# Optimization experiments

Measured on AMD Instinct MI355X. Metric: run time of the kernel, lower is better.

The kernel has to match this reference:

```python
import jax, jax.numpy as jnp
import numpy as np

B, C, H, W = 8, 256, 128, 128
CQ = C // 8  # query/key channel dim = 32


def setup_inputs() -> dict:
    key = jax.random.key(0)
    ks = jax.random.split(key, 8)
    s = 0.05
    return {
        "x": jax.random.normal(ks[0], (B, C, H, W), jnp.float32),
        "Wq": jax.random.normal(ks[1], (CQ, C), jnp.float32) * s,
        "bq": jax.random.normal(ks[2], (CQ,), jnp.float32) * s,
        "Wk": jax.random.normal(ks[3], (CQ, C), jnp.float32) * s,
        "bk": jax.random.normal(ks[4], (CQ,), jnp.float32) * s,
        "Wv": jax.random.normal(ks[5], (C, C), jnp.float32) * s,
        "bv": jax.random.normal(ks[6], (C,), jnp.float32) * s,
        "gamma": jax.random.normal(ks[7], (1,), jnp.float32),
    }


def reference(x, Wq, bq, Wk, bk, Wv, bv, gamma):
    b, c, h, w = x.shape
    # 1x1 convs == channel-mixing einsums
    q = jnp.einsum('oc,bchw->bohw', Wq, x) + bq[None, :, None, None]   # [B,CQ,H,W]
    k = jnp.einsum('oc,bchw->bohw', Wk, x) + bk[None, :, None, None]   # [B,CQ,H,W]
    v = jnp.einsum('oc,bchw->bohw', Wv, x) + bv[None, :, None, None]   # [B,C,H,W]
    # energy along height: for each column w, attend over rows g; -inf on diagonal
    eH = jnp.einsum('bohw,bogw->bhwg', q, k)                            # [B,H,W,H]
    diag = jnp.eye(h, dtype=bool)                                       # h==g
    eH = jnp.where(diag[None, :, None, :], -jnp.inf, eH)
    # energy along width: for each row h, attend over columns g
    eW = jnp.einsum('bohw,bohg->bhwg', q, k)                            # [B,H,W,W]
    att = jax.nn.softmax(jnp.concatenate([eH, eW], axis=-1), axis=-1)   # [B,H,W,H+W]
    aH, aW = att[..., :h], att[..., h:]
    outH = jnp.einsum('bhwg,bcgw->bchw', aH, v)
    outW = jnp.einsum('bhwg,bchg->bchw', aW, v)
    return gamma[0] * (outH + outW) + x
```

## Files before the change

kernel.cpp:

```cpp
#include <hip/hip_runtime.h>
#include <math.h>

#define B 8
#define C 256
#define CQ 32
#define H 128
#define W 128
#define P (H*W)

typedef unsigned short ushortT;
typedef __attribute__((ext_vector_type(8))) short bf16x8;
typedef __attribute__((ext_vector_type(4))) float f32x4;

__device__ __forceinline__ float bf2f(ushortT u) {
    union { unsigned int i; float f; } v; v.i = ((unsigned int)u) << 16; return v.f;
}
__device__ __forceinline__ ushortT f2bf(float f) {
    union { float f; unsigned int i; } v; v.f = f;
    unsigned int u = v.i;
    unsigned int r = (u + 0x7FFFu + ((u >> 16) & 1u)) >> 16;
    return (ushortT)r;
}

__global__ void pack_kernel(
    const float* __restrict__ Wq, const float* __restrict__ bq,
    const float* __restrict__ Wk, const float* __restrict__ bk,
    const float* __restrict__ Wv, const float* __restrict__ bv,
    ushortT* __restrict__ Wall, float* __restrict__ biasAll)
{
    const int t = threadIdx.x;
    if (blockIdx.x == 80) {
        for (int i = t; i < 320; i += 256) {
            float bv_;
            if (i < 32)       bv_ = bq[i];
            else if (i < 64)  bv_ = bk[i - 32];
            else              bv_ = bv[i - 64];
            biasAll[i] = bv_;
        }
        return;
    }
    int g = blockIdx.x * 256 + t;
    int idx4 = g * 4;
    int row = idx4 >> 8, col = idx4 & 255;
    const float* src;
    if (row < 32)       src = Wq + (size_t)row * 256 + col;
    else if (row < 64)  src = Wk + (size_t)(row - 32) * 256 + col;
    else                src = Wv + (size_t)(row - 64) * 256 + col;
    float4 v4 = *(const float4*)src;
    ushort4 u;
    u.x = f2bf(v4.x); u.y = f2bf(v4.y); u.z = f2bf(v4.z); u.w = f2bf(v4.w);
    *(ushort4*)(Wall + idx4) = u;
}

__global__ __launch_bounds__(256) void proj_mfma(
    const float* __restrict__ x, const ushortT* __restrict__ Wall,
    const float* __restrict__ biasAll,
    ushortT* __restrict__ qb, ushortT* __restrict__ kb, ushortT* __restrict__ vb)
{
    __shared__ ushortT Xs[64][264];
    const int t  = threadIdx.x;
    const int p0 = blockIdx.x * 64;
    const int b  = blockIdx.y;

    {
        const float* xb = x + (size_t)b * C * P + p0;
        int c = t >> 4, pq = (t & 15) * 4;
        #pragma unroll
        for (int i = 0; i < 16; i++) {
            int ci = c + i * 16;
            float4 v4 = *(const float4*)(xb + (size_t)ci * P + pq);
            Xs[pq + 0][ci] = f2bf(v4.x);
            Xs[pq + 1][ci] = f2bf(v4.y);
            Xs[pq + 2][ci] = f2bf(v4.z);
            Xs[pq + 3][ci] = f2bf(v4.w);
        }
    }
    __syncthreads();

    const int wid = t >> 6, lane = t & 63;
    const int lrow = lane & 15, lk = (lane >> 4) * 8;

    f32x4 acc[5][4];
    #pragma unroll
    for (int mi = 0; mi < 5; mi++)
        #pragma unroll
        for (int ni = 0; ni < 4; ni++)
            acc[mi][ni] = (f32x4){0.f, 0.f, 0.f, 0.f};

    const ushortT* wbase = Wall + (size_t)(wid * 80 + lrow) * 256 + lk;

    #pragma unroll
    for (int kk = 0; kk < 8; kk++) {
        bf16x8 a[5], bfr[4];
        #pragma unroll
        for (int mi = 0; mi < 5; mi++)
            a[mi] = *(const bf16x8*)(wbase + mi * 16 * 256 + kk * 32);
        #pragma unroll
        for (int ni = 0; ni < 4; ni++)
            bfr[ni] = *(const bf16x8*)&Xs[ni * 16 + lrow][kk * 32 + lk];
        #pragma unroll
        for (int mi = 0; mi < 5; mi++)
            #pragma unroll
            for (int ni = 0; ni < 4; ni++)
                acc[mi][ni] = __builtin_amdgcn_mfma_f32_16x16x32_bf16(
                    a[mi], bfr[ni], acc[mi][ni], 0, 0, 0);
    }

    const int orow0 = wid * 80 + (lane >> 4) * 4;
    #pragma unroll
    for (int mi = 0; mi < 5; mi++) {
        #pragma unroll
        for (int reg = 0; reg < 4; reg++) {
            int o = orow0 + mi * 16 + reg;
            float bias = biasAll[o];
            ushortT* dst;
            if (o < 32)      dst = qb + ((size_t)(b * CQ + o)) * P;
            else if (o < 64) dst = kb + ((size_t)(b * CQ + o - 32)) * P;
            else             dst = vb + ((size_t)(b * C + o - 64)) * P;
            #pragma unroll
            for (int ni = 0; ni < 4; ni++)
                dst[p0 + ni * 16 + lrow] = f2bf(acc[mi][ni][reg] + bias);
        }
    }
}

__global__ void transpose_v_kernel(const ushortT* __restrict__ vb, ushortT* __restrict__ vt)
{
    __shared__ ushortT tile[32][33];
    const int w0 = blockIdx.x * 32, h0 = blockIdx.y * 32;
    const int bc = blockIdx.z;
    const int b = bc >> 8, c = bc & 255;
    const int txx = threadIdx.x;
    const ushortT* src = vb + (size_t)bc * P;
    for (int r = threadIdx.y; r < 32; r += 8)
        tile[r][txx] = src[(size_t)(h0 + r) * W + w0 + txx];
    __syncthreads();
    for (int r = threadIdx.y; r < 32; r += 8) {
        size_t didx = (((size_t)b * W + (w0 + r)) * C + c) * H + h0 + txx;
        vt[didx] = tile[txx][r];
    }
}

__global__ __launch_bounds__(256) void eh_kernel(
    const ushortT* __restrict__ qb, const ushortT* __restrict__ kb, ushortT* __restrict__ att)
{
    __shared__ float Qs[CQ][132];
    __shared__ float Ks[CQ][132];
    const int t = threadIdx.x;
    const int w = blockIdx.x, b = blockIdx.y;
    #pragma unroll
    for (int i = 0; i < 16; i++) {
        int idx = i * 256 + t;
        int o = idx >> 7, h = idx & 127;
        size_t g = ((size_t)(b * CQ + o)) * P + (size_t)h * W + w;
        Qs[o][h] = bf2f(qb[g]);
        Ks[o][h] = bf2f(kb[g]);
    }
    __syncthreads();
    const int hb = t >> 5;
    const int gq = (t & 31) * 4;
    const float NEGINF = -__builtin_inff();
    for (int pass = 0; pass < 16; pass++) {
        int h = pass * 8 + hb;
        float qr[CQ];
        #pragma unroll
        for (int o = 0; o < CQ; o++) qr[o] = Qs[o][h];
        float4 a = {0.f, 0.f, 0.f, 0.f};
        #pragma unroll
        for (int o = 0; o < CQ; o++) {
            float4 kv = *(const float4*)&Ks[o][gq];
            a.x = fmaf(qr[o], kv.x, a.x);
            a.y = fmaf(qr[o], kv.y, a.y);
            a.z = fmaf(qr[o], kv.z, a.z);
            a.w = fmaf(qr[o], kv.w, a.w);
        }
        if (gq     == h) a.x = NEGINF;
        if (gq + 1 == h) a.y = NEGINF;
        if (gq + 2 == h) a.z = NEGINF;
        if (gq + 3 == h) a.w = NEGINF;
        ushort4 u;
        u.x = f2bf(a.x); u.y = f2bf(a.y); u.z = f2bf(a.z); u.w = f2bf(a.w);
        *(ushort4*)&att[((size_t)(b * P + h * W + w)) * 256 + gq] = u;
    }
}

__global__ __launch_bounds__(256) void ew_kernel(
    const ushortT* __restrict__ qb, const ushortT* __restrict__ kb, ushortT* __restrict__ att)
{
    __shared__ float Qs[CQ][132];
    __shared__ float Ks[CQ][132];
    const int t = threadIdx.x;
    const int h = blockIdx.x, b = blockIdx.y;
    #pragma unroll
    for (int r = 0; r < 4; r++) {
        int qd = r * 256 + t;
        int o = qd >> 5, wq = (qd & 31) * 4;
        size_t g = ((size_t)(b * CQ + o)) * P + (size_t)h * W + wq;
        ushort4 qv = *(const ushort4*)&qb[g];
        ushort4 kv = *(const ushort4*)&kb[g];
        Qs[o][wq + 0] = bf2f(qv.x); Qs[o][wq + 1] = bf2f(qv.y);
        Qs[o][wq + 2] = bf2f(qv.z); Qs[o][wq + 3] = bf2f(qv.w);
        Ks[o][wq + 0] = bf2f(kv.x); Ks[o][wq + 1] = bf2f(kv.y);
        Ks[o][wq + 2] = bf2f(kv.z); Ks[o][wq + 3] = bf2f(kv.w);
    }
    __syncthreads();
    const int wb = t >> 5;
    const int gq = (t & 31) * 4;
    for (int pass = 0; pass < 16; pass++) {
        int w = pass * 8 + wb;
        float qr[CQ];
        #pragma unroll
        for (int o = 0; o < CQ; o++) qr[o] = Qs[o][w];
        float4 a = {0.f, 0.f, 0.f, 0.f};
        #pragma unroll
        for (int o = 0; o < CQ; o++) {
            float4 kv = *(const float4*)&Ks[o][gq];
            a.x = fmaf(qr[o], kv.x, a.x);
            a.y = fmaf(qr[o], kv.y, a.y);
            a.z = fmaf(qr[o], kv.z, a.z);
            a.w = fmaf(qr[o], kv.w, a.w);
        }
        ushort4 u;
        u.x = f2bf(a.x); u.y = f2bf(a.y); u.z = f2bf(a.z); u.w = f2bf(a.w);
        *(ushort4*)&att[((size_t)(b * P + h * W + w)) * 256 + 128 + gq] = u;
    }
}

__global__ void softmax_kernel(ushortT* __restrict__ att)
{
    const int t = threadIdx.x;
    const int r = t >> 6, lane = t & 63;
    size_t pix = (size_t)blockIdx.x * 4 + r;
    ushort4* row = (ushort4*)(att + pix * 256);
    ushort4 u = row[lane];
    float v0 = bf2f(u.x), v1 = bf2f(u.y), v2 = bf2f(u.z), v3 = bf2f(u.w);
    float m = fmaxf(fmaxf(v0, v1), fmaxf(v2, v3));
    #pragma unroll
    for (int off = 32; off; off >>= 1) m = fmaxf(m, __shfl_xor(m, off));
    float e0 = __expf(v0 - m), e1 = __expf(v1 - m);
    float e2 = __expf(v2 - m), e3 = __expf(v3 - m);
    float s = e0 + e1 + e2 + e3;
    #pragma unroll
    for (int off = 32; off; off >>= 1) s += __shfl_xor(s, off);
    float inv = 1.f / s;
    u.x = f2bf(e0 * inv); u.y = f2bf(e1 * inv);
    u.z = f2bf(e2 * inv); u.w = f2bf(e3 * inv);
    row[lane] = u;
}

__global__ __launch_bounds__(256) void outh_mfma(
    ushortT* __restrict__ vt, const ushortT* __restrict__ att)
{
    __shared__ ushortT Vs[128 * 128];
    __shared__ ushortT Ats[128 * 128];
    const int t = threadIdx.x;
    const int c0 = blockIdx.x * 128;
    const int w = blockIdx.y, b = blockIdx.z;

    const ushortT* vsrc = vt + (((size_t)b * W + w) * C + c0) * H;
    const ushortT* asrc = att + ((size_t)b * P + w) * 256;
    #pragma unroll
    for (int i = 0; i < 8; i++) {
        int q = i * 256 + t;
        int row = q >> 4, c8 = (q & 15) * 8;
        int sidx = (row * 128 + c8) ^ ((row & 7) << 3);
        *(bf16x8*)&Vs[sidx]  = *(const bf16x8*)(vsrc + (size_t)row * 128 + c8);
        *(bf16x8*)&Ats[sidx] = *(const bf16x8*)(asrc + (size_t)row * (W * 256) + c8);
    }
    __syncthreads();

    const int wid = t >> 6, lane = t & 63;
    const int wm = wid >> 1, wn = wid & 1;
    const int lrow = lane & 15, lk8 = (lane >> 4) * 8;

    f32x4 acc[4][4];
    #pragma unroll
    for (int mi = 0; mi < 4; mi++)
        #pragma unroll
        for (int ni = 0; ni < 4; ni++)
            acc[mi][ni] = (f32x4){0.f, 0.f, 0.f, 0.f};

    #pragma unroll
    for (int kk = 0; kk < 4; kk++) {
        bf16x8 a[4], bb[4];
        #pragma unroll
        for (int mi = 0; mi < 4; mi++) {
            int r = wm * 64 + mi * 16 + lrow;
            a[mi] = *(const bf16x8*)&Vs[(r * 128 + kk * 32 + lk8) ^ ((r & 7) << 3)];
        }
        #pragma unroll
        for (int ni = 0; ni < 4; ni++) {
            int r = wn * 64 + ni * 16 + lrow;
            bb[ni] = *(const bf16x8*)&Ats[(r * 128 + kk * 32 + lk8) ^ ((r & 7) << 3)];
        }
        #pragma unroll
        for (int mi = 0; mi < 4; mi++)
            #pragma unroll
            for (int ni = 0; ni < 4; ni++)
                acc[mi][ni] = __builtin_amdgcn_mfma_f32_16x16x32_bf16(
                    a[mi], bb[ni], acc[mi][ni], 0, 0, 0);
    }

    ushortT* dst = vt + (((size_t)b * W + w) * C + c0) * H;
    #pragma unroll
    for (int mi = 0; mi < 4; mi++)
        #pragma unroll
        for (int reg = 0; reg < 4; reg++) {
            int cc = wm * 64 + mi * 16 + (lane >> 4) * 4 + reg;
            #pragma unroll
            for (int ni = 0; ni < 4; ni++) {
                int hh = wn * 64 + ni * 16 + lrow;
                dst[(size_t)cc * 128 + hh] = f2bf(acc[mi][ni][reg]);
            }
        }
}

__global__ __launch_bounds__(256) void outw_mfma(
    const ushortT* __restrict__ vb, const ushortT* __restrict__ att, float* __restrict__ out)
{
    __shared__ ushortT Vs[128 * 128];
    __shared__ ushortT Ats[128 * 128];
    const int t = threadIdx.x;
    const int c0 = blockIdx.x * 128;
    const int h = blockIdx.y, b = blockIdx.z;

    const ushortT* vsrc = vb + ((size_t)(b * C + c0)) * P + (size_t)h * W;
    const ushortT* asrc = att + ((size_t)b * P + (size_t)h * W) * 256 + 128;
    #pragma unroll
    for (int i = 0; i < 8; i++) {
        int q = i * 256 + t;
        int row = q >> 4, c8 = (q & 15) * 8;
        int sidx = (row * 128 + c8) ^ ((row & 7) << 3);
        *(bf16x8*)&Vs[sidx]  = *(const bf16x8*)(vsrc + (size_t)row * P + c8);
        *(bf16x8*)&Ats[sidx] = *(const bf16x8*)(asrc + (size_t)row * 256 + c8);
    }
    __syncthreads();

    const int wid = t >> 6, lane = t & 63;
    const int wm = wid >> 1, wn = wid & 1;
    const int lrow = lane & 15, lk8 = (lane >> 4) * 8;

    f32x4 acc[4][4];
    #pragma unroll
    for (int mi = 0; mi < 4; mi++)
        #pragma unroll
        for (int ni = 0; ni < 4; ni++)
            acc[mi][ni] = (f32x4){0.f, 0.f, 0.f, 0.f};

    #pragma unroll
    for (int kk = 0; kk < 4; kk++) {
        bf16x8 a[4], bb[4];
        #pragma unroll
        for (int mi = 0; mi < 4; mi++) {
            int r = wm * 64 + mi * 16 + lrow;
            a[mi] = *(const bf16x8*)&Vs[(r * 128 + kk * 32 + lk8) ^ ((r & 7) << 3)];
        }
        #pragma unroll
        for (int ni = 0; ni < 4; ni++) {
            int r = wn * 64 + ni * 16 + lrow;
            bb[ni] = *(const bf16x8*)&Ats[(r * 128 + kk * 32 + lk8) ^ ((r & 7) << 3)];
        }
        #pragma unroll
        for (int mi = 0; mi < 4; mi++)
            #pragma unroll
            for (int ni = 0; ni < 4; ni++)
                acc[mi][ni] = __builtin_amdgcn_mfma_f32_16x16x32_bf16(
                    a[mi], bb[ni], acc[mi][ni], 0, 0, 0);
    }

    #pragma unroll
    for (int mi = 0; mi < 4; mi++)
        #pragma unroll
        for (int reg = 0; reg < 4; reg++) {
            int cc = c0 + wm * 64 + mi * 16 + (lane >> 4) * 4 + reg;
            #pragma unroll
            for (int ni = 0; ni < 4; ni++) {
                int ww = wn * 64 + ni * 16 + lrow;
                out[((size_t)(b * C + cc)) * P + (size_t)h * W + ww] = acc[mi][ni][reg];
            }
        }
}

__global__ void combine_kernel(
    const ushortT* __restrict__ oht, const float* __restrict__ x,
    const float* __restrict__ gamma, float* __restrict__ out)
{
    __shared__ ushortT tile[32][33];
    const int t = threadIdx.x;
    const int w0 = blockIdx.x * 32, h0 = blockIdx.y * 32;
    const int bc = blockIdx.z;
    const int b = bc >> 8, c = bc & 255;
    const int r = t >> 3, cq = (t & 7) * 4;

    const ushortT* src = oht + (((size_t)b * W + w0 + r) * C + c) * H + h0 + cq;
    ushort4 v = *(const ushort4*)src;
    tile[r][cq + 0] = v.x; tile[r][cq + 1] = v.y;
    tile[r][cq + 2] = v.z; tile[r][cq + 3] = v.w;
    __syncthreads();

    const float g = gamma[0];
    size_t idx = ((size_t)bc) * P + (size_t)(h0 + r) * W + w0 + cq;
    float4 ov = *(const float4*)&out[idx];
    float4 xv = *(const float4*)&x[idx];
    float4 res;
    res.x = g * (ov.x + bf2f(tile[cq + 0][r])) + xv.x;
    res.y = g * (ov.y + bf2f(tile[cq + 1][r])) + xv.y;
    res.z = g * (ov.z + bf2f(tile[cq + 2][r])) + xv.z;
    res.w = g * (ov.w + bf2f(tile[cq + 3][r])) + xv.w;
    *(float4*)&out[idx] = res;
}

extern "C" void kernel_launch(void* const* d_in, const int* in_sizes, int n_in,
                              void* d_out, int out_size, void* d_ws, size_t ws_size,
                              hipStream_t stream)
{
    const float* x     = (const float*)d_in[0];
    const float* Wq    = (const float*)d_in[1];
    const float* bq    = (const float*)d_in[2];
    const float* Wk    = (const float*)d_in[3];
    const float* bk    = (const float*)d_in[4];
    const float* Wv    = (const float*)d_in[5];
    const float* bv    = (const float*)d_in[6];
    const float* gamma = (const float*)d_in[7];
    float* out = (float*)d_out;

    ushortT* ws = (ushortT*)d_ws;
    const size_t qk_sz  = (size_t)B * CQ * P;
    const size_t v_sz   = (size_t)B * C  * P;
    const size_t att_sz = (size_t)B * P * 256;

    ushortT* qb  = ws;
    ushortT* kb  = qb  + qk_sz;
    ushortT* vb  = kb  + qk_sz;
    ushortT* vto = vb  + v_sz;
    ushortT* att = vto + v_sz;

    ushortT* Wall   = att;
    float*   biasAll = (float*)(att + 81920);

    const size_t needed_bytes = (2 * qk_sz + 2 * v_sz + att_sz) * sizeof(ushortT);
    if (ws_size < needed_bytes) return;

    pack_kernel<<<dim3(81), 256, 0, stream>>>(Wq, bq, Wk, bk, Wv, bv, Wall, biasAll);
    proj_mfma<<<dim3(P / 64, B), 256, 0, stream>>>(x, Wall, biasAll, qb, kb, vb);
    transpose_v_kernel<<<dim3(W / 32, H / 32, B * C), dim3(32, 8), 0, stream>>>(vb, vto);
    eh_kernel<<<dim3(W, B), 256, 0, stream>>>(qb, kb, att);
    ew_kernel<<<dim3(H, B), 256, 0, stream>>>(qb, kb, att);
    softmax_kernel<<<dim3(B * P / 4), 256, 0, stream>>>(att);
    outh_mfma<<<dim3(2, W, B), 256, 0, stream>>>(vto, att);
    outw_mfma<<<dim3(2, H, B), 256, 0, stream>>>(vb, att, out);
    combine_kernel<<<dim3(W / 32, H / 32, B * C), 256, 0, stream>>>(vto, x, gamma, out);
}
```

Baseline: 620.9 us.

## Use MFMA for energy kernels, fuse softmax into ew, coalesce stores via LDS staging

Energy computations along height and width now run on bf16 MFMA, reading q/k from new pixel-major layouts produced by the projection kernel. The softmax is folded into the width-energy kernel, which removes one full pass over the attention buffer. The projection now takes a pre-transposed bf16 x from a separate transpose kernel and weights prepacked into MFMA fragment order, with a larger pixel tile. Epilogues of the projection and both output GEMMs stage results through LDS so that global stores are vectorized. The trade-off is an extra transpose kernel, more LDS use and register pressure, and the energies are still rounded to bf16 before the softmax.

```diff
diff --git a/kernel.cpp b/kernel.cpp
--- a/kernel.cpp
+++ b/kernel.cpp
@@ -26,10 +26,10 @@
     const float* __restrict__ Wq, const float* __restrict__ bq,
     const float* __restrict__ Wk, const float* __restrict__ bk,
     const float* __restrict__ Wv, const float* __restrict__ bv,
-    ushortT* __restrict__ Wall, float* __restrict__ biasAll)
-{
-    const int t = threadIdx.x;
-    if (blockIdx.x == 80) {
+    ushortT* __restrict__ Wfrag, float* __restrict__ biasAll)
+{
+    const int t = threadIdx.x;
+    if (blockIdx.x == 40) {
         for (int i = t; i < 320; i += 256) {
             float bv_;
             if (i < 32)       bv_ = bq[i];
@@ -40,87 +40,151 @@
         return;
     }
     int g = blockIdx.x * 256 + t;
-    int idx4 = g * 4;
-    int row = idx4 >> 8, col = idx4 & 255;
+    int f = g >> 6, lane = g & 63;
+    int widp = f / 40, rem = f % 40;
+    int kk = rem / 5, mi = rem % 5;
+    int orow = (widp * 5 + mi) * 16 + (lane & 15);
+    int col  = kk * 32 + (lane >> 4) * 8;
     const float* src;
-    if (row < 32)       src = Wq + (size_t)row * 256 + col;
-    else if (row < 64)  src = Wk + (size_t)(row - 32) * 256 + col;
-    else                src = Wv + (size_t)(row - 64) * 256 + col;
-    float4 v4 = *(const float4*)src;
-    ushort4 u;
-    u.x = f2bf(v4.x); u.y = f2bf(v4.y); u.z = f2bf(v4.z); u.w = f2bf(v4.w);
-    *(ushort4*)(Wall + idx4) = u;
-}
-
-__global__ __launch_bounds__(256) void proj_mfma(
-    const float* __restrict__ x, const ushortT* __restrict__ Wall,
+    if (orow < 32)      src = Wq + (size_t)orow * C + col;
+    else if (orow < 64) src = Wk + (size_t)(orow - 32) * C + col;
+    else                src = Wv + (size_t)(orow - 64) * C + col;
+    float4 v0 = *(const float4*)src;
+    float4 v1 = *(const float4*)(src + 4);
+    bf16x8 o;
+    o[0] = (short)f2bf(v0.x); o[1] = (short)f2bf(v0.y);
+    o[2] = (short)f2bf(v0.z); o[3] = (short)f2bf(v0.w);
+    o[4] = (short)f2bf(v1.x); o[5] = (short)f2bf(v1.y);
+    o[6] = (short)f2bf(v1.z); o[7] = (short)f2bf(v1.w);
+    *(bf16x8*)(Wfrag + (size_t)g * 8) = o;
+}
+
+__global__ void xt_kernel(const float* __restrict__ x, ushortT* __restrict__ xt)
+{
+    __shared__ ushortT tile[32][72];
+    const int t = threadIdx.x;
+    const int p0 = blockIdx.x * 32, c0 = blockIdx.y * 64;
+    const int b = blockIdx.z;
+    #pragma unroll
+    for (int j = 0; j < 8; j++) {
+        int q = j * 256 + t;
+        int cr = q >> 5, pc = q & 31;
+        tile[pc][cr] = f2bf(x[((size_t)b * C + c0 + cr) * P + p0 + pc]);
+    }
+    __syncthreads();
+    {
+        int pr = t >> 3, c8 = (t & 7) * 8;
+        bf16x8 v;
+        #pragma unroll
+        for (int i = 0; i < 8; i++) v[i] = (short)tile[pr][c8 + i];
+        *(bf16x8*)&xt[((size_t)b * P + p0 + pr) * C + c0 + c8] = v;
+    }
+}
+
+__global__ __launch_bounds__(256, 2) void proj_mfma(
+    const ushortT* __restrict__ xt, const ushortT* __restrict__ Wfrag,
     const float* __restrict__ biasAll,
-    ushortT* __restrict__ qb, ushortT* __restrict__ kb, ushortT* __restrict__ vb)
-{
-    __shared__ ushortT Xs[64][264];
-    const int t  = threadIdx.x;
-    const int p0 = blockIdx.x * 64;
-    const int b  = blockIdx.y;
+    ushortT* __restrict__ qt, ushortT* __restrict__ kt, ushortT* __restrict__ vb)
+{
+    __shared__ ushortT smem[32768];
+    const int t = threadIdx.x;
+    const int p0 = blockIdx.x * 128;
+    const int b = blockIdx.y;
+    const int wid = t >> 6, lane = t & 63;
+    const int lrow = lane & 15, lk8 = (lane >> 4) * 8;
+    const int hi4 = (lane >> 4) * 4;
 
     {
-        const float* xb = x + (size_t)b * C * P + p0;
-        int c = t >> 4, pq = (t & 15) * 4;
-        #pragma unroll
-        for (int i = 0; i < 16; i++) {
-            int ci = c + i * 16;
-            float4 v4 = *(const float4*)(xb + (size_t)ci * P + pq);
-            Xs[pq + 0][ci] = f2bf(v4.x);
-            Xs[pq + 1][ci] = f2bf(v4.y);
-            Xs[pq + 2][ci] = f2bf(v4.z);
-            Xs[pq + 3][ci] = f2bf(v4.w);
-        }
-    }
-    __syncthreads();
-
-    const int wid = t >> 6, lane = t & 63;
-    const int lrow = lane & 15, lk = (lane >> 4) * 8;
-
-    f32x4 acc[5][4];
+        const ushortT* xtb = xt + ((size_t)b * P + p0) * 256;
+        #pragma unroll
+        for (int j = 0; j < 16; j++) {
+            int q = j * 256 + t;
+            int off = q * 8;
+            int px = off >> 8, cu = off & 255;
+            bf16x8 val = *(const bf16x8*)(xtb + (size_t)px * 256 + cu);
+            *(bf16x8*)&smem[px * 256 + (cu ^ ((px & 7) << 3))] = val;
+        }
+    }
+    __syncthreads();
+
+    f32x4 acc[5][8];
     #pragma unroll
     for (int mi = 0; mi < 5; mi++)
         #pragma unroll
-        for (int ni = 0; ni < 4; ni++)
+        for (int ni = 0; ni < 8; ni++)
             acc[mi][ni] = (f32x4){0.f, 0.f, 0.f, 0.f};
 
-    const ushortT* wbase = Wall + (size_t)(wid * 80 + lrow) * 256 + lk;
-
-    #pragma unroll
+    const int sw = (lrow & 7) << 3;
+    #pragma unroll 1
     for (int kk = 0; kk < 8; kk++) {
-        bf16x8 a[5], bfr[4];
+        bf16x8 a[5], bb[8];
         #pragma unroll
         for (int mi = 0; mi < 5; mi++)
-            a[mi] = *(const bf16x8*)(wbase + mi * 16 * 256 + kk * 32);
-        #pragma unroll
-        for (int ni = 0; ni < 4; ni++)
-            bfr[ni] = *(const bf16x8*)&Xs[ni * 16 + lrow][kk * 32 + lk];
+            a[mi] = *(const bf16x8*)(Wfrag +
+                ((size_t)(((wid * 8 + kk) * 5 + mi) * 64 + lane) << 3));
+        #pragma unroll
+        for (int ni = 0; ni < 8; ni++)
+            bb[ni] = *(const bf16x8*)&smem[(ni * 16 + lrow) * 256 +
+                ((kk * 32 + lk8) ^ sw)];
         #pragma unroll
         for (int mi = 0; mi < 5; mi++)
             #pragma unroll
-            for (int ni = 0; ni < 4; ni++)
+            for (int ni = 0; ni < 8; ni++)
                 acc[mi][ni] = __builtin_amdgcn_mfma_f32_16x16x32_bf16(
-                    a[mi], bfr[ni], acc[mi][ni], 0, 0, 0);
-    }
-
-    const int orow0 = wid * 80 + (lane >> 4) * 4;
-    #pragma unroll
-    for (int mi = 0; mi < 5; mi++) {
-        #pragma unroll
-        for (int reg = 0; reg < 4; reg++) {
-            int o = orow0 + mi * 16 + reg;
-            float bias = biasAll[o];
-            ushortT* dst;
-            if (o < 32)      dst = qb + ((size_t)(b * CQ + o)) * P;
-            else if (o < 64) dst = kb + ((size_t)(b * CQ + o - 32)) * P;
-            else             dst = vb + ((size_t)(b * C + o - 64)) * P;
-            #pragma unroll
-            for (int ni = 0; ni < 4; ni++)
-                dst[p0 + ni * 16 + lrow] = f2bf(acc[mi][ni][reg] + bias);
-        }
+                    a[mi], bb[ni], acc[mi][ni], 0, 0, 0);
+    }
+    __syncthreads();
+
+    ushortT* S = smem;
+    for (int ph = 0; ph < 2; ph++) {
+        if ((wid >> 1) == ph) {
+            #pragma unroll
+            for (int mi = 0; mi < 5; mi++)
+                #pragma unroll
+                for (int reg = 0; reg < 4; reg++) {
+                    int o = wid * 80 + mi * 16 + hi4 + reg;
+                    int ol = o - ph * 160;
+                    float bias = biasAll[o];
+                    #pragma unroll
+                    for (int ni = 0; ni < 8; ni++)
+                        S[ol * 136 + ni * 16 + lrow] = f2bf(acc[mi][ni][reg] + bias);
+                }
+        }
+        __syncthreads();
+        if (ph == 0) {
+            {
+                int px = t >> 1, oh = (t & 1) * 16;
+                size_t pixbase = ((size_t)b * P + p0 + px) * 32 + oh;
+                bf16x8 q0, q1, k0, k1;
+                #pragma unroll
+                for (int i = 0; i < 8; i++) {
+                    q0[i] = (short)S[(oh + i) * 136 + px];
+                    q1[i] = (short)S[(oh + 8 + i) * 136 + px];
+                    k0[i] = (short)S[(32 + oh + i) * 136 + px];
+                    k1[i] = (short)S[(32 + oh + 8 + i) * 136 + px];
+                }
+                *(bf16x8*)&qt[pixbase]     = q0;
+                *(bf16x8*)&qt[pixbase + 8] = q1;
+                *(bf16x8*)&kt[pixbase]     = k0;
+                *(bf16x8*)&kt[pixbase + 8] = k1;
+            }
+            #pragma unroll
+            for (int j = 0; j < 6; j++) {
+                int q = j * 256 + t;
+                int row = q >> 4, c8 = (q & 15) * 8;
+                bf16x8 v = *(const bf16x8*)&S[(64 + row) * 136 + c8];
+                *(bf16x8*)&vb[((size_t)b * C + row) * P + p0 + c8] = v;
+            }
+        } else {
+            #pragma unroll
+            for (int j = 0; j < 10; j++) {
+                int q = j * 256 + t;
+                int row = q >> 4, c8 = (q & 15) * 8;
+                bf16x8 v = *(const bf16x8*)&S[row * 136 + c8];
+                *(bf16x8*)&vb[((size_t)b * C + 96 + row) * P + p0 + c8] = v;
+            }
+        }
+        __syncthreads();
     }
 }
 
@@ -141,118 +205,134 @@
     }
 }
 
-__global__ __launch_bounds__(256) void eh_kernel(
-    const ushortT* __restrict__ qb, const ushortT* __restrict__ kb, ushortT* __restrict__ att)
-{
-    __shared__ float Qs[CQ][132];
-    __shared__ float Ks[CQ][132];
+__global__ __launch_bounds__(256) void eh_mfma(
+    const ushortT* __restrict__ qt, const ushortT* __restrict__ kt, ushortT* __restrict__ att)
+{
+    __shared__ ushortT S[128 * 136];
     const int t = threadIdx.x;
     const int w = blockIdx.x, b = blockIdx.y;
-    #pragma unroll
-    for (int i = 0; i < 16; i++) {
-        int idx = i * 256 + t;
-        int o = idx >> 7, h = idx & 127;
-        size_t g = ((size_t)(b * CQ + o)) * P + (size_t)h * W + w;
-        Qs[o][h] = bf2f(qb[g]);
-        Ks[o][h] = bf2f(kb[g]);
-    }
-    __syncthreads();
-    const int hb = t >> 5;
-    const int gq = (t & 31) * 4;
-    const float NEGINF = -__builtin_inff();
-    for (int pass = 0; pass < 16; pass++) {
-        int h = pass * 8 + hb;
-        float qr[CQ];
-        #pragma unroll
-        for (int o = 0; o < CQ; o++) qr[o] = Qs[o][h];
-        float4 a = {0.f, 0.f, 0.f, 0.f};
-        #pragma unroll
-        for (int o = 0; o < CQ; o++) {
-            float4 kv = *(const float4*)&Ks[o][gq];
-            a.x = fmaf(qr[o], kv.x, a.x);
-            a.y = fmaf(qr[o], kv.y, a.y);
-            a.z = fmaf(qr[o], kv.z, a.z);
-            a.w = fmaf(qr[o], kv.w, a.w);
-        }
-        if (gq     == h) a.x = NEGINF;
-        if (gq + 1 == h) a.y = NEGINF;
-        if (gq + 2 == h) a.z = NEGINF;
-        if (gq + 3 == h) a.w = NEGINF;
-        ushort4 u;
-        u.x = f2bf(a.x); u.y = f2bf(a.y); u.z = f2bf(a.z); u.w = f2bf(a.w);
-        *(ushort4*)&att[((size_t)(b * P + h * W + w)) * 256 + gq] = u;
-    }
-}
-
-__global__ __launch_bounds__(256) void ew_kernel(
-    const ushortT* __restrict__ qb, const ushortT* __restrict__ kb, ushortT* __restrict__ att)
-{
-    __shared__ float Qs[CQ][132];
-    __shared__ float Ks[CQ][132];
+    const int wid = t >> 6, lane = t & 63;
+    const int lrow = lane & 15, lk8 = (lane >> 4) * 8;
+    const int hi4 = (lane >> 4) * 4;
+    const ushortT* qtb = qt + (size_t)b * P * 32;
+    const ushortT* ktb = kt + (size_t)b * P * 32;
+
+    bf16x8 a[2], bb[8];
+    #pragma unroll
+    for (int mi = 0; mi < 2; mi++) {
+        int h = wid * 32 + mi * 16 + lrow;
+        a[mi] = *(const bf16x8*)&qtb[((size_t)(h * W + w)) * 32 + lk8];
+    }
+    #pragma unroll
+    for (int ni = 0; ni < 8; ni++) {
+        int g = ni * 16 + lrow;
+        bb[ni] = *(const bf16x8*)&ktb[((size_t)(g * W + w)) * 32 + lk8];
+    }
+    f32x4 acc[2][8];
+    #pragma unroll
+    for (int mi = 0; mi < 2; mi++)
+        #pragma unroll
+        for (int ni = 0; ni < 8; ni++)
+            acc[mi][ni] = __builtin_amdgcn_mfma_f32_16x16x32_bf16(
+                a[mi], bb[ni], (f32x4){0.f, 0.f, 0.f, 0.f}, 0, 0, 0);
+
+    #pragma unroll
+    for (int mi = 0; mi < 2; mi++)
+        #pragma unroll
+        for (int reg = 0; reg < 4; reg++) {
+            int h = wid * 32 + mi * 16 + hi4 + reg;
+            #pragma unroll
+            for (int ni = 0; ni < 8; ni++) {
+                int g = ni * 16 + lrow;
+                S[h * 136 + g] = (g == h) ? (ushortT)0xFF80 : f2bf(acc[mi][ni][reg]);
+            }
+        }
+    __syncthreads();
+    #pragma unroll
+    for (int j = 0; j < 8; j++) {
+        int q = j * 256 + t;
+        int row = q >> 4, c8 = (q & 15) * 8;
+        bf16x8 v = *(const bf16x8*)&S[row * 136 + c8];
+        *(bf16x8*)&att[((size_t)b * P + row * W + w) * 256 + c8] = v;
+    }
+}
+
+__global__ __launch_bounds__(256) void ew_sm(
+    const ushortT* __restrict__ qt, const ushortT* __restrict__ kt, ushortT* __restrict__ att)
+{
+    __shared__ ushortT eWs[128 * 136];
     const int t = threadIdx.x;
     const int h = blockIdx.x, b = blockIdx.y;
-    #pragma unroll
-    for (int r = 0; r < 4; r++) {
-        int qd = r * 256 + t;
-        int o = qd >> 5, wq = (qd & 31) * 4;
-        size_t g = ((size_t)(b * CQ + o)) * P + (size_t)h * W + wq;
-        ushort4 qv = *(const ushort4*)&qb[g];
-        ushort4 kv = *(const ushort4*)&kb[g];
-        Qs[o][wq + 0] = bf2f(qv.x); Qs[o][wq + 1] = bf2f(qv.y);
-        Qs[o][wq + 2] = bf2f(qv.z); Qs[o][wq + 3] = bf2f(qv.w);
-        Ks[o][wq + 0] = bf2f(kv.x); Ks[o][wq + 1] = bf2f(kv.y);
-        Ks[o][wq + 2] = bf2f(kv.z); Ks[o][wq + 3] = bf2f(kv.w);
-    }
-    __syncthreads();
-    const int wb = t >> 5;
-    const int gq = (t & 31) * 4;
-    for (int pass = 0; pass < 16; pass++) {
-        int w = pass * 8 + wb;
-        float qr[CQ];
-        #pragma unroll
-        for (int o = 0; o < CQ; o++) qr[o] = Qs[o][w];
-        float4 a = {0.f, 0.f, 0.f, 0.f};
-        #pragma unroll
-        for (int o = 0; o < CQ; o++) {
-            float4 kv = *(const float4*)&Ks[o][gq];
-            a.x = fmaf(qr[o], kv.x, a.x);
-            a.y = fmaf(qr[o], kv.y, a.y);
-            a.z = fmaf(qr[o], kv.z, a.z);
-            a.w = fmaf(qr[o], kv.w, a.w);
-        }
-        ushort4 u;
-        u.x = f2bf(a.x); u.y = f2bf(a.y); u.z = f2bf(a.z); u.w = f2bf(a.w);
-        *(ushort4*)&att[((size_t)(b * P + h * W + w)) * 256 + 128 + gq] = u;
-    }
-}
-
-__global__ void softmax_kernel(ushortT* __restrict__ att)
-{
-    const int t = threadIdx.x;
-    const int r = t >> 6, lane = t & 63;
-    size_t pix = (size_t)blockIdx.x * 4 + r;
-    ushort4* row = (ushort4*)(att + pix * 256);
-    ushort4 u = row[lane];
-    float v0 = bf2f(u.x), v1 = bf2f(u.y), v2 = bf2f(u.z), v3 = bf2f(u.w);
-    float m = fmaxf(fmaxf(v0, v1), fmaxf(v2, v3));
-    #pragma unroll
-    for (int off = 32; off; off >>= 1) m = fmaxf(m, __shfl_xor(m, off));
-    float e0 = __expf(v0 - m), e1 = __expf(v1 - m);
-    float e2 = __expf(v2 - m), e3 = __expf(v3 - m);
-    float s = e0 + e1 + e2 + e3;
-    #pragma unroll
-    for (int off = 32; off; off >>= 1) s += __shfl_xor(s, off);
-    float inv = 1.f / s;
-    u.x = f2bf(e0 * inv); u.y = f2bf(e1 * inv);
-    u.z = f2bf(e2 * inv); u.w = f2bf(e3 * inv);
-    row[lane] = u;
+    const int wid = t >> 6, lane = t & 63;
+    const int lrow = lane & 15, lk8 = (lane >> 4) * 8;
+    const int hi4 = (lane >> 4) * 4;
+    const ushortT* qtb = qt + (size_t)b * P * 32;
+    const ushortT* ktb = kt + (size_t)b * P * 32;
+
+    bf16x8 a[2], bb[8];
+    #pragma unroll
+    for (int mi = 0; mi < 2; mi++) {
+        int wr = wid * 32 + mi * 16 + lrow;
+        a[mi] = *(const bf16x8*)&qtb[((size_t)(h * W + wr)) * 32 + lk8];
+    }
+    #pragma unroll
+    for (int ni = 0; ni < 8; ni++) {
+        int g = ni * 16 + lrow;
+        bb[ni] = *(const bf16x8*)&ktb[((size_t)(h * W + g)) * 32 + lk8];
+    }
+    f32x4 acc[2][8];
+    #pragma unroll
+    for (int mi = 0; mi < 2; mi++)
+        #pragma unroll
+        for (int ni = 0; ni < 8; ni++)
+            acc[mi][ni] = __builtin_amdgcn_mfma_f32_16x16x32_bf16(
+                a[mi], bb[ni], (f32x4){0.f, 0.f, 0.f, 0.f}, 0, 0, 0);
+
+    #pragma unroll
+    for (int mi = 0; mi < 2; mi++)
+        #pragma unroll
+        for (int reg = 0; reg < 4; reg++) {
+            int wl = wid * 32 + mi * 16 + hi4 + reg;
+            #pragma unroll
+            for (int ni = 0; ni < 8; ni++)
+                eWs[wl * 136 + ni * 16 + lrow] = f2bf(acc[mi][ni][reg]);
+        }
+    __syncthreads();
+
+    for (int r = 0; r < 32; r++) {
+        int wl = wid * 32 + r;
+        size_t pix = (size_t)b * P + h * W + wl;
+        ushortT* rowp = att + pix * 256;
+        float v0, v1, v2, v3;
+        if (lane < 32) {
+            ushort4 u = *(const ushort4*)&rowp[lane * 4];
+            v0 = bf2f(u.x); v1 = bf2f(u.y); v2 = bf2f(u.z); v3 = bf2f(u.w);
+        } else {
+            ushort4 u = *(const ushort4*)&eWs[wl * 136 + (lane - 32) * 4];
+            v0 = bf2f(u.x); v1 = bf2f(u.y); v2 = bf2f(u.z); v3 = bf2f(u.w);
+        }
+        float m = fmaxf(fmaxf(v0, v1), fmaxf(v2, v3));
+        #pragma unroll
+        for (int off = 32; off; off >>= 1) m = fmaxf(m, __shfl_xor(m, off));
+        float e0 = __expf(v0 - m), e1 = __expf(v1 - m);
+        float e2 = __expf(v2 - m), e3 = __expf(v3 - m);
+        float s = e0 + e1 + e2 + e3;
+        #pragma unroll
+        for (int off = 32; off; off >>= 1) s += __shfl_xor(s, off);
+        float inv = 1.f / s;
+        ushort4 o;
+        o.x = f2bf(e0 * inv); o.y = f2bf(e1 * inv);
+        o.z = f2bf(e2 * inv); o.w = f2bf(e3 * inv);
+        *(ushort4*)&rowp[lane * 4] = o;
+    }
 }
 
 __global__ __launch_bounds__(256) void outh_mfma(
     ushortT* __restrict__ vt, const ushortT* __restrict__ att)
 {
-    __shared__ ushortT Vs[128 * 128];
-    __shared__ ushortT Ats[128 * 128];
+    __shared__ ushortT smem[32768];
+    ushortT* Vs  = smem;
+    ushortT* Ats = smem + 16384;
     const int t = threadIdx.x;
     const int c0 = blockIdx.x * 128;
     const int w = blockIdx.y, b = blockIdx.z;
@@ -272,6 +352,7 @@
     const int wid = t >> 6, lane = t & 63;
     const int wm = wid >> 1, wn = wid & 1;
     const int lrow = lane & 15, lk8 = (lane >> 4) * 8;
+    const int hi4 = (lane >> 4) * 4;
 
     f32x4 acc[4][4];
     #pragma unroll
@@ -300,26 +381,36 @@
                 acc[mi][ni] = __builtin_amdgcn_mfma_f32_16x16x32_bf16(
                     a[mi], bb[ni], acc[mi][ni], 0, 0, 0);
     }
-
+    __syncthreads();
+
+    ushortT* S = smem;
+    #pragma unroll
+    for (int mi = 0; mi < 4; mi++)
+        #pragma unroll
+        for (int reg = 0; reg < 4; reg++) {
+            int cl = wm * 64 + mi * 16 + hi4 + reg;
+            #pragma unroll
+            for (int ni = 0; ni < 4; ni++) {
+                int hl = wn * 64 + ni * 16 + lrow;
+                S[cl * 136 + hl] = f2bf(acc[mi][ni][reg]);
+            }
+        }
+    __syncthreads();
     ushortT* dst = vt + (((size_t)b * W + w) * C + c0) * H;
     #pragma unroll
-    for (int mi = 0; mi < 4; mi++)
-        #pragma unroll
-        for (int reg = 0; reg < 4; reg++) {
-            int cc = wm * 64 + mi * 16 + (lane >> 4) * 4 + reg;
-            #pragma unroll
-            for (int ni = 0; ni < 4; ni++) {
-                int hh = wn * 64 + ni * 16 + lrow;
-                dst[(size_t)cc * 128 + hh] = f2bf(acc[mi][ni][reg]);
-            }
-        }
+    for (int j = 0; j < 8; j++) {
+        int q = j * 256 + t;
+        int row = q >> 4, c8 = (q & 15) * 8;
+        *(bf16x8*)&dst[(size_t)row * H + c8] = *(const bf16x8*)&S[row * 136 + c8];
+    }
 }
 
 __global__ __launch_bounds__(256) void outw_mfma(
     const ushortT* __restrict__ vb, const ushortT* __restrict__ att, float* __restrict__ out)
 {
-    __shared__ ushortT Vs[128 * 128];
-    __shared__ ushortT Ats[128 * 128];
+    __shared__ ushortT smem[32768];
+    ushortT* Vs  = smem;
+    ushortT* Ats = smem + 16384;
     const int t = threadIdx.x;
     const int c0 = blockIdx.x * 128;
     const int h = blockIdx.y, b = blockIdx.z;
@@ -339,6 +430,7 @@
     const int wid = t >> 6, lane = t & 63;
     const int wm = wid >> 1, wn = wid & 1;
     const int lrow = lane & 15, lk8 = (lane >> 4) * 8;
+    const int hi4 = (lane >> 4) * 4;
 
     f32x4 acc[4][4];
     #pragma unroll
@@ -367,18 +459,33 @@
                 acc[mi][ni] = __builtin_amdgcn_mfma_f32_16x16x32_bf16(
                     a[mi], bb[ni], acc[mi][ni], 0, 0, 0);
     }
-
-    #pragma unroll
-    for (int mi = 0; mi < 4; mi++)
-        #pragma unroll
-        for (int reg = 0; reg < 4; reg++) {
-            int cc = c0 + wm * 64 + mi * 16 + (lane >> 4) * 4 + reg;
-            #pragma unroll
-            for (int ni = 0; ni < 4; ni++) {
-                int ww = wn * 64 + ni * 16 + lrow;
-                out[((size_t)(b * C + cc)) * P + (size_t)h * W + ww] = acc[mi][ni][reg];
-            }
-        }
+    __syncthreads();
+
+    float* S = (float*)smem;
+    for (int ph = 0; ph < 2; ph++) {
+        if (wm == ph) {
+            #pragma unroll
+            for (int mi = 0; mi < 4; mi++)
+                #pragma unroll
+                for (int reg = 0; reg < 4; reg++) {
+                    int cl = mi * 16 + hi4 + reg;
+                    #pragma unroll
+                    for (int ni = 0; ni < 4; ni++) {
+                        int hl = wn * 64 + ni * 16 + lrow;
+                        S[cl * 132 + hl] = acc[mi][ni][reg];
+                    }
+                }
+        }
+        __syncthreads();
+        #pragma unroll
+        for (int j = 0; j < 8; j++) {
+            int q = j * 256 + t;
+            int row = q >> 5, f4 = (q & 31) * 4;
+            float4 v = *(const float4*)&S[row * 132 + f4];
+            *(float4*)&out[((size_t)b * C + c0 + ph * 64 + row) * P + (size_t)h * W + f4] = v;
+        }
+        __syncthreads();
+    }
 }
 
 __global__ void combine_kernel(
@@ -429,24 +536,25 @@
     const size_t v_sz   = (size_t)B * C  * P;
     const size_t att_sz = (size_t)B * P * 256;
 
-    ushortT* qb  = ws;
-    ushortT* kb  = qb  + qk_sz;
-    ushortT* vb  = kb  + qk_sz;
+    ushortT* qt  = ws;
+    ushortT* kt  = qt  + qk_sz;
+    ushortT* vb  = kt  + qk_sz;
     ushortT* vto = vb  + v_sz;
     ushortT* att = vto + v_sz;
 
-    ushortT* Wall   = att;
+    ushortT* xt     = vto;
+    ushortT* Wfrag  = att;
     float*   biasAll = (float*)(att + 81920);
 
     const size_t needed_bytes = (2 * qk_sz + 2 * v_sz + att_sz) * sizeof(ushortT);
     if (ws_size < needed_bytes) return;
 
-    pack_kernel<<<dim3(81), 256, 0, stream>>>(Wq, bq, Wk, bk, Wv, bv, Wall, biasAll);
-    proj_mfma<<<dim3(P / 64, B), 256, 0, stream>>>(x, Wall, biasAll, qb, kb, vb);
+    pack_kernel<<<dim3(41), 256, 0, stream>>>(Wq, bq, Wk, bk, Wv, bv, Wfrag, biasAll);
+    xt_kernel<<<dim3(P / 32, C / 64, B), 256, 0, stream>>>(x, xt);
+    proj_mfma<<<dim3(P / 128, B), 256, 0, stream>>>(xt, Wfrag, biasAll, qt, kt, vb);
     transpose_v_kernel<<<dim3(W / 32, H / 32, B * C), dim3(32, 8), 0, stream>>>(vb, vto);
-    eh_kernel<<<dim3(W, B), 256, 0, stream>>>(qb, kb, att);
-    ew_kernel<<<dim3(H, B), 256, 0, stream>>>(qb, kb, att);
-    softmax_kernel<<<dim3(B * P / 4), 256, 0, stream>>>(att);
+    eh_mfma<<<dim3(W, B), 256, 0, stream>>>(qt, kt, att);
+    ew_sm<<<dim3(H, B), 256, 0, stream>>>(qt, kt, att);
     outh_mfma<<<dim3(2, W, B), 256, 0, stream>>>(vto, att);
     outw_mfma<<<dim3(2, H, B), 256, 0, stream>>>(vb, att, out);
     combine_kernel<<<dim3(W / 32, H / 32, B * C), 256, 0, stream>>>(vto, x, gamma, out);
```

Result: faster. 525.1 us (-15.4%).
